# Performance work log

Measured on AMD Instinct MI355X. Metric: run time of the kernel, lower is better.

The kernel has to match this reference:

```python
import jax, jax.numpy as jnp
import numpy as np

B, S, D = 2, 4096, 256
H, DH, DM = 8, 32, 1024
ROPE_BASE = 10000.0
LN_EPS = 1e-5


def _layer_norm(x, g, b):
    mu = jnp.mean(x, axis=-1, keepdims=True)
    var = jnp.mean(jnp.square(x - mu), axis=-1, keepdims=True)
    return (x - mu) * jax.lax.rsqrt(var + LN_EPS) * g + b


def _rope(x):
    # x: [b, s, h, d_head]; lucidrains interleaved-pair RoPE
    s, d = x.shape[1], x.shape[-1]
    inv_freq = 1.0 / (ROPE_BASE ** (jnp.arange(0, d, 2, dtype=jnp.float32) / d))  # [d/2]
    freqs = jnp.arange(s, dtype=jnp.float32)[:, None] * inv_freq[None, :]          # [s, d/2]
    freqs = jnp.repeat(freqs, 2, axis=-1)                                          # [s, d]
    cos = jnp.cos(freqs)[None, :, None, :]
    sin = jnp.sin(freqs)[None, :, None, :]
    x1, x2 = x[..., 0::2], x[..., 1::2]
    rot = jnp.stack((-x2, x1), axis=-1).reshape(x.shape)
    return x * cos + rot * sin


def setup_inputs() -> dict:
    key = jax.random.key(0)
    ks = jax.random.split(key, 8)
    sw = 1.0 / np.sqrt(D)
    return {
        "x": jax.random.normal(ks[0], (B, S, D), jnp.float32),
        "Wq": jax.random.normal(ks[1], (D, D), jnp.float32) * sw,
        "Wk": jax.random.normal(ks[2], (D, D), jnp.float32) * sw,
        "Wv": jax.random.normal(ks[3], (D, D), jnp.float32) * sw,
        "Wo": jax.random.normal(ks[4], (D, D), jnp.float32) * sw,
        "ln1_g": jnp.ones((D,), jnp.float32),
        "ln1_b": jnp.zeros((D,), jnp.float32),
        "ln2_g": jnp.ones((D,), jnp.float32),
        "ln2_b": jnp.zeros((D,), jnp.float32),
        "W2": jax.random.normal(ks[5], (DM, D), jnp.float32) * sw,
        "b2": jnp.zeros((DM,), jnp.float32),
        "W3": jax.random.normal(ks[6], (D, DM), jnp.float32) * (1.0 / np.sqrt(DM)),
        "b3": jnp.zeros((D,), jnp.float32),
    }


def reference(x, Wq, Wk, Wv, Wo, ln1_g, ln1_b, ln2_g, ln2_b, W2, b2, W3, b3):
    b, s, d = x.shape
    h, dh = H, DH
    xn = _layer_norm(x, ln1_g, ln1_b)
    q = (xn @ Wq.T).reshape(b, s, h, dh)
    k = (xn @ Wk.T).reshape(b, s, h, dh)
    v = (xn @ Wv.T).reshape(b, s, h, dh)
    q = _rope(q)
    k = _rope(k)
    # scores: [b, h, q, k] (full matrix, matching original implementation)
    scores = jnp.einsum('bqhd,bkhd->bhqk', q, k) / np.sqrt(dh)
    attn = jax.nn.softmax(scores, axis=-1)
    out = jnp.einsum('bhqk,bkhd->bqhd', attn, v).reshape(b, s, d)
    out = out @ Wo.T
    mlp_in = out + x
    y = _layer_norm(mlp_in, ln2_g, ln2_b)
    y = jax.nn.gelu(y @ W2.T + b2, approximate=False)
    y = y @ W3.T + b3
    return y + mlp_in
```

## Files before the change

### kernel.cpp

```cpp
#include <hip/hip_runtime.h>
#include <math.h>

#define D 256
#define S 4096
#define H 8
#define DH 32
#define DM 1024
#define NTOK 8192

typedef __attribute__((ext_vector_type(8))) short short8;
typedef __attribute__((ext_vector_type(4))) float f32x4;

#define QSCALE (0.17677669529663687f * 1.4426950408889634f)

__device__ inline unsigned short f2bf(float f) {
    union { float f; unsigned u; } v; v.f = f;
    unsigned r = v.u + 0x7fffu + ((v.u >> 16) & 1u);
    return (unsigned short)(r >> 16);
}
__device__ inline void gload16(const void* g, void* l) {
    __builtin_amdgcn_global_load_lds((const __attribute__((address_space(1))) void*)g,
                                     (__attribute__((address_space(3))) void*)l, 16, 0, 0);
}

__global__ void prep(const float* __restrict__ Wq, const float* __restrict__ Wk,
                     const float* __restrict__ Wv, const float* __restrict__ Wo,
                     const float* __restrict__ W2, const float* __restrict__ W3,
                     unsigned short* __restrict__ wqkv, unsigned short* __restrict__ wo_b,
                     unsigned short* __restrict__ w2_b, unsigned short* __restrict__ w3_b,
                     float* __restrict__ ct, float* __restrict__ st,
                     const float* __restrict__ x, const float* __restrict__ g,
                     const float* __restrict__ b, unsigned short* __restrict__ xn) {
    int blk = blockIdx.x;
    if (blk < 3328) {
        int i = blk * 256 + threadIdx.x;
        if (i < 196608) {
            const float* s = (i < 65536) ? Wq : ((i < 131072) ? Wk : Wv);
            wqkv[i] = f2bf(s[i & 65535]);
        } else if (i < 262144) {
            wo_b[i - 196608] = f2bf(Wo[i - 196608]);
        } else if (i < 524288) {
            w2_b[i - 262144] = f2bf(W2[i - 262144]);
        } else if (i < 786432) {
            w3_b[i - 524288] = f2bf(W3[i - 524288]);
        } else {
            int j = i - 786432;
            int spos = j >> 4, pi = j & 15;
            float inv_freq = powf(10000.0f, -(float)(2 * pi) / 32.0f);
            float fr = (float)spos * inv_freq;
            ct[j] = cosf(fr);
            st[j] = sinf(fr);
        }
        return;
    }
    int l = threadIdx.x & 63;
    int row = (blk - 3328) * 4 + (threadIdx.x >> 6);
    const float4 v = *(const float4*)(x + (size_t)row * D + l * 4);
    float s  = v.x + v.y + v.z + v.w;
    float s2 = v.x * v.x + v.y * v.y + v.z * v.z + v.w * v.w;
    #pragma unroll
    for (int off = 32; off > 0; off >>= 1) {
        s  += __shfl_xor(s, off, 64);
        s2 += __shfl_xor(s2, off, 64);
    }
    float mu  = s * (1.0f / D);
    float var = s2 * (1.0f / D) - mu * mu;
    float rs  = rsqrtf(var + 1e-5f);
    const float4 gg = *(const float4*)(g + l * 4);
    const float4 bb = *(const float4*)(b + l * 4);
    ushort4 o;
    o.x = f2bf((v.x - mu) * rs * gg.x + bb.x);
    o.y = f2bf((v.y - mu) * rs * gg.y + bb.y);
    o.z = f2bf((v.z - mu) * rs * gg.z + bb.z);
    o.w = f2bf((v.w - mu) * rs * gg.w + bb.w);
    *(ushort4*)(xn + (size_t)row * D + l * 4) = o;
}

__global__ void ln_kernel(const float* __restrict__ x, const float* __restrict__ g,
                          const float* __restrict__ b, unsigned short* __restrict__ out) {
    int l = threadIdx.x & 63;
    int row = blockIdx.x * 4 + (threadIdx.x >> 6);
    const float4 v = *(const float4*)(x + (size_t)row * D + l * 4);
    float s  = v.x + v.y + v.z + v.w;
    float s2 = v.x * v.x + v.y * v.y + v.z * v.z + v.w * v.w;
    #pragma unroll
    for (int off = 32; off > 0; off >>= 1) {
        s  += __shfl_xor(s, off, 64);
        s2 += __shfl_xor(s2, off, 64);
    }
    float mu  = s * (1.0f / D);
    float var = s2 * (1.0f / D) - mu * mu;
    float rs  = rsqrtf(var + 1e-5f);
    const float4 gg = *(const float4*)(g + l * 4);
    const float4 bb = *(const float4*)(b + l * 4);
    ushort4 o;
    o.x = f2bf((v.x - mu) * rs * gg.x + bb.x);
    o.y = f2bf((v.y - mu) * rs * gg.y + bb.y);
    o.z = f2bf((v.z - mu) * rs * gg.z + bb.z);
    o.w = f2bf((v.w - mu) * rs * gg.w + bb.w);
    *(ushort4*)(out + (size_t)row * D + l * 4) = o;
}

__global__ __launch_bounds__(256) void gemm64b(const unsigned short* __restrict__ A,
        const unsigned short* __restrict__ Bw, void* __restrict__ outp,
        unsigned short* __restrict__ vt,
        const float* __restrict__ bias,
        const float* __restrict__ ct, const float* __restrict__ st,
        int N, int K, int mode) {
    __shared__ unsigned short As[2][64 * 64];
    __shared__ unsigned short Bs[2][64 * 64];
    int tid = threadIdx.x;
    int w = tid >> 6, l = tid & 63;
    int lm = l & 15, lg = l >> 4;
    int wm = (w >> 1) * 32, wn = (w & 1) * 32;
    int bm = blockIdx.x * 64, bn = blockIdx.y * 64;
    int r1 = tid >> 3, pc = tid & 7;
    int pcx = (pc ^ (r1 & 7)) * 8;
    const unsigned short* Ag1 = A + (size_t)(bm + r1) * K + pcx;
    const unsigned short* Ag2 = A + (size_t)(bm + 32 + r1) * K + pcx;
    const unsigned short* Bg1 = Bw + (size_t)(bn + r1) * K + pcx;
    const unsigned short* Bg2 = Bw + (size_t)(bn + 32 + r1) * K + pcx;
    const int swz = lm & 7;
    f32x4 acc[2][2] = {};

    gload16(Ag1, &As[0][w * 512]);
    gload16(Ag2, &As[0][2048 + w * 512]);
    gload16(Bg1, &Bs[0][w * 512]);
    gload16(Bg2, &Bs[0][2048 + w * 512]);
    for (int k0 = 0; k0 < K; k0 += 64) {
        int cur = (k0 >> 6) & 1;
        __syncthreads();
        if (k0 + 64 < K) {
            gload16(Ag1 + k0 + 64, &As[1 - cur][w * 512]);
            gload16(Ag2 + k0 + 64, &As[1 - cur][2048 + w * 512]);
            gload16(Bg1 + k0 + 64, &Bs[1 - cur][w * 512]);
            gload16(Bg2 + k0 + 64, &Bs[1 - cur][2048 + w * 512]);
        }
        #pragma unroll
        for (int j = 0; j < 2; ++j) {
            int ch = ((j * 4 + lg) ^ swz) * 8;
            short8 af[2], bf[2];
            #pragma unroll
            for (int i = 0; i < 2; ++i) af[i] = *(const short8*)&As[cur][(wm + i * 16 + lm) * 64 + ch];
            #pragma unroll
            for (int i = 0; i < 2; ++i) bf[i] = *(const short8*)&Bs[cur][(wn + i * 16 + lm) * 64 + ch];
            #pragma unroll
            for (int mi = 0; mi < 2; ++mi)
                #pragma unroll
                for (int ni = 0; ni < 2; ++ni)
                    acc[mi][ni] = __builtin_amdgcn_mfma_f32_16x16x32_bf16(af[mi], bf[ni], acc[mi][ni], 0, 0, 0);
        }
    }

    if (mode == 0) {
        if (bn >= 512) {
            #pragma unroll
            for (int mi = 0; mi < 2; ++mi) {
                #pragma unroll
                for (int ni = 0; ni < 2; ++ni) {
                    int ng = bn + wn + ni * 16 + lm - 512;
                    int hh = ng >> 5, dh = ng & 31;
                    int mg0 = bm + wm + mi * 16 + lg * 4;
                    int bb = mg0 >> 12, ss = mg0 & 4095;
                    ushort4 pv;
                    pv.x = f2bf(acc[mi][ni][0]); pv.y = f2bf(acc[mi][ni][1]);
                    pv.z = f2bf(acc[mi][ni][2]); pv.w = f2bf(acc[mi][ni][3]);
                    *(ushort4*)(vt + ((size_t)((bb * 8 + hh) * 32 + dh)) * S + ss) = pv;
                }
            }
        } else {
            #pragma unroll
            for (int mi = 0; mi < 2; ++mi) {
                #pragma unroll
                for (int ni = 0; ni < 2; ++ni) {
                    int ng = bn + wn + ni * 16 + lm;
                    int pi = (ng & 31) >> 1;
                    float sgn = (ng & 1) ? 1.f : -1.f;
                    float qs  = (ng < 256) ? QSCALE : 1.f;
                    #pragma unroll
                    for (int r2 = 0; r2 < 4; ++r2) {
                        int mg = bm + wm + mi * 16 + lg * 4 + r2;
                        int spos = mg & (S - 1);
                        float vv = acc[mi][ni][r2];
                        float pv = __shfl_xor(vv, 1, 64);
                        float cs = ct[spos * 16 + pi];
                        float sn = st[spos * 16 + pi];
                        float ov = (vv * cs + sgn * pv * sn) * qs;
                        ((unsigned short*)outp)[(size_t)mg * N + ng] = f2bf(ov);
                    }
                }
            }
        }
        return;
    }
    #pragma unroll
    for (int mi = 0; mi < 2; ++mi) {
        #pragma unroll
        for (int ni = 0; ni < 2; ++ni) {
            int ng = bn + wn + ni * 16 + lm;
            #pragma unroll
            for (int r2 = 0; r2 < 4; ++r2) {
                int mg = bm + wm + mi * 16 + lg * 4 + r2;
                float t = acc[mi][ni][r2] + bias[ng];
                ((unsigned short*)outp)[(size_t)mg * N + ng] =
                    f2bf(0.5f * t * (1.0f + erff(t * 0.70710678118654752f)));
            }
        }
    }
}

__global__ __launch_bounds__(256) void gemm32(const unsigned short* __restrict__ A,
        const unsigned short* __restrict__ Bw, void* __restrict__ outp,
        const float* __restrict__ bias, const float* __restrict__ res,
        int N, int K, int mode) {
    __shared__ unsigned short As[2][32 * 128];
    __shared__ unsigned short Bs[2][64 * 128];
    int tid = threadIdx.x;
    int w = tid >> 6, l = tid & 63;
    int lm = l & 15, lg = l >> 4;
    int rm = (w >> 1) * 16, wn = (w & 1) * 32;
    int bm = blockIdx.x * 32, bn = blockIdx.y * 64;
    int r1 = tid >> 4, pc = tid & 15;
    int pcx = (pc ^ (r1 & 7)) * 8;
    const unsigned short* Ag1 = A + (size_t)(bm + r1) * K + pcx;
    const unsigned short* Ag2 = A + (size_t)(bm + 16 + r1) * K + pcx;
    const unsigned short* Bg1 = Bw + (size_t)(bn + r1) * K + pcx;
    const unsigned short* Bg2 = Bw + (size_t)(bn + 16 + r1) * K + pcx;
    const unsigned short* Bg3 = Bw + (size_t)(bn + 32 + r1) * K + pcx;
    const unsigned short* Bg4 = Bw + (size_t)(bn + 48 + r1) * K + pcx;
    const int swz = lm & 7;
    f32x4 acc[2] = {};

    gload16(Ag1, &As[0][w * 512]);
    gload16(Ag2, &As[0][2048 + w * 512]);
    gload16(Bg1, &Bs[0][w * 512]);
    gload16(Bg2, &Bs[0][2048 + w * 512]);
    gload16(Bg3, &Bs[0][4096 + w * 512]);
    gload16(Bg4, &Bs[0][6144 + w * 512]);
    for (int k0 = 0; k0 < K; k0 += 128) {
        int cur = (k0 >> 7) & 1;
        __syncthreads();
        if (k0 + 128 < K) {
            gload16(Ag1 + k0 + 128, &As[1 - cur][w * 512]);
            gload16(Ag2 + k0 + 128, &As[1 - cur][2048 + w * 512]);
            gload16(Bg1 + k0 + 128, &Bs[1 - cur][w * 512]);
            gload16(Bg2 + k0 + 128, &Bs[1 - cur][2048 + w * 512]);
            gload16(Bg3 + k0 + 128, &Bs[1 - cur][4096 + w * 512]);
            gload16(Bg4 + k0 + 128, &Bs[1 - cur][6144 + w * 512]);
        }
        #pragma unroll
        for (int j = 0; j < 4; ++j) {
            int ch = ((j * 4 + lg) ^ swz) * 8;
            short8 af = *(const short8*)&As[cur][(rm + lm) * 128 + ch];
            short8 bf[2];
            #pragma unroll
            for (int i = 0; i < 2; ++i) bf[i] = *(const short8*)&Bs[cur][(wn + i * 16 + lm) * 128 + ch];
            #pragma unroll
            for (int ni = 0; ni < 2; ++ni)
                acc[ni] = __builtin_amdgcn_mfma_f32_16x16x32_bf16(af, bf[ni], acc[ni], 0, 0, 0);
        }
    }

    #pragma unroll
    for (int ni = 0; ni < 2; ++ni) {
        int ng = bn + wn + ni * 16 + lm;
        #pragma unroll
        for (int r2 = 0; r2 < 4; ++r2) {
            int mg = bm + rm + lg * 4 + r2;
            float v = acc[ni][r2];
            size_t idx = (size_t)mg * N + ng;
            if (mode == 1) {
                ((float*)outp)[idx] = v + res[idx];
            } else {
                ((float*)outp)[idx] = v + bias[ng] + res[idx];
            }
        }
    }
}

__global__ __launch_bounds__(512) void attn_kernel(const unsigned short* __restrict__ Cq,
        const unsigned short* __restrict__ vt, unsigned short* __restrict__ out) {
    __shared__ unsigned short Ks[2][2][64][32];
    __shared__ unsigned short Vs[2][2][32][64];
    __shared__ unsigned short Ones[16][64];
    int tid = threadIdx.x;
    int w = tid >> 6, l = tid & 63;
    int grp = w >> 2, ws = w & 3;
    int lm = l & 15, lg = l >> 4;
    int qt = blockIdx.x >> 4;
    int bh = blockIdx.x & 15;
    int bb = bh >> 3, h = bh & 7;
    int q0 = qt * 64 + ws * 16;

    if (tid < 256) {
        unsigned short val = (tid < 16) ? (unsigned short)0x3F80 : (unsigned short)0;
        *(ushort4*)(&Ones[0][0] + tid * 4) = make_ushort4(val, val, val, val);
    }

    const short8 qf = *(const short8*)(Cq + ((size_t)(bb * S + q0 + lm)) * 768 + h * DH + lg * 8);
    int p = ws * 16 + (l >> 2);
    int krow = ((p >> 5) << 5) + (((p >> 2) & 3) << 3) + (((p >> 4) & 1) << 2) + (p & 3);
    const unsigned short* kg = Cq + ((size_t)(bb * S)) * 768 + 256 + h * 32
                               + (size_t)krow * 768 + ((l & 3) ^ ((l >> 3) & 3)) * 8;
    const unsigned short* vg = vt + ((size_t)(bh * 32 + ws * 8 + (l >> 3))) * S + ((l & 7) ^ (l >> 3)) * 8;
    const int kswz = (lm >> 1) & 3;
    const int vswz = lm & 7;

    f32x4 o0 = {0.f, 0.f, 0.f, 0.f}, o1 = {0.f, 0.f, 0.f, 0.f}, o2 = {0.f, 0.f, 0.f, 0.f};
    const f32x4 z = {0.f, 0.f, 0.f, 0.f};

    gload16(kg + (size_t)grp * 64 * 768, &Ks[grp][0][ws * 16][0]);
    gload16(vg + (size_t)grp * 64,       &Vs[grp][0][ws * 8][0]);

    #pragma unroll 2
    for (int it = 0; it < S / 128; ++it) {
        int cur = it & 1;
        __syncthreads();
        if (it + 1 < S / 128) {
            size_t t = (size_t)(2 * (it + 1) + grp);
            gload16(kg + t * 64 * 768, &Ks[grp][1 - cur][ws * 16][0]);
            gload16(vg + t * 64,       &Vs[grp][1 - cur][ws * 8][0]);
        }
        #pragma unroll
        for (int half = 0; half < 2; ++half) {
            short8 kf0 = *(const short8*)&Ks[grp][cur][half * 32 + lm][(lg ^ kswz) * 8];
            short8 kf1 = *(const short8*)&Ks[grp][cur][half * 32 + 16 + lm][(lg ^ kswz) * 8];
            f32x4 s0 = __builtin_amdgcn_mfma_f32_16x16x32_bf16(kf0, qf, z, 0, 0, 0);
            f32x4 s1 = __builtin_amdgcn_mfma_f32_16x16x32_bf16(kf1, qf, z, 0, 0, 0);
            unsigned u0[4], u1[4];
            #pragma unroll
            for (int i = 0; i < 4; ++i) {
                union { float f; unsigned u; } c0, c1;
                c0.f = __builtin_amdgcn_exp2f(s0[i]);
                c1.f = __builtin_amdgcn_exp2f(s1[i]);
                u0[i] = c0.u;
                u1[i] = c1.u;
            }
            union { unsigned u[4]; short8 s; } pk;
            pk.u[0] = __builtin_amdgcn_perm(u0[1], u0[0], 0x07060302u);
            pk.u[1] = __builtin_amdgcn_perm(u0[3], u0[2], 0x07060302u);
            pk.u[2] = __builtin_amdgcn_perm(u1[1], u1[0], 0x07060302u);
            pk.u[3] = __builtin_amdgcn_perm(u1[3], u1[2], 0x07060302u);
            short8 pf = pk.s;
            int vc = ((half * 4 + lg) ^ vswz) * 8;
            short8 va0 = *(const short8*)&Vs[grp][cur][lm][vc];
            short8 va1 = *(const short8*)&Vs[grp][cur][16 + lm][vc];
            short8 va2 = *(const short8*)&Ones[lm][vc];
            o0 = __builtin_amdgcn_mfma_f32_16x16x32_bf16(va0, pf, o0, 0, 0, 0);
            o1 = __builtin_amdgcn_mfma_f32_16x16x32_bf16(va1, pf, o1, 0, 0, 0);
            o2 = __builtin_amdgcn_mfma_f32_16x16x32_bf16(va2, pf, o2, 0, 0, 0);
        }
    }
    f32x4* Red0 = (f32x4*)&Ks[1][0][0][0];
    f32x4* Red1 = (f32x4*)&Vs[1][0][0][0];
    float* Den  = (float*)&Ones[0][0];
    __syncthreads();
    if (grp) {
        Red0[ws * 64 + l] = o0;
        Red1[ws * 64 + l] = o1;
        Den[ws * 64 + l]  = o2[0];
    }
    __syncthreads();
    if (!grp) {
        f32x4 a0 = Red0[ws * 64 + l];
        f32x4 a1 = Red1[ws * 64 + l];
        float dd = o2[0] + Den[ws * 64 + l];
        #pragma unroll
        for (int i = 0; i < 4; ++i) { o0[i] += a0[i]; o1[i] += a1[i]; }
        float lsum = __shfl(dd, lm, 64);
        float inv = 1.0f / lsum;
        ushort4 r0, r1;
        r0.x = f2bf(o0[0] * inv); r0.y = f2bf(o0[1] * inv);
        r0.z = f2bf(o0[2] * inv); r0.w = f2bf(o0[3] * inv);
        r1.x = f2bf(o1[0] * inv); r1.y = f2bf(o1[1] * inv);
        r1.z = f2bf(o1[2] * inv); r1.w = f2bf(o1[3] * inv);
        unsigned short* ob = out + ((size_t)(bb * S + q0 + lm)) * D + h * DH;
        *(ushort4*)(ob + lg * 4)      = r0;
        *(ushort4*)(ob + 16 + lg * 4) = r1;
    }
}

extern "C" void kernel_launch(void* const* d_in, const int* in_sizes, int n_in,
                              void* d_out, int out_size, void* d_ws, size_t ws_size,
                              hipStream_t stream) {
    const float* x     = (const float*)d_in[0];
    const float* Wq    = (const float*)d_in[1];
    const float* Wk    = (const float*)d_in[2];
    const float* Wv    = (const float*)d_in[3];
    const float* Wo    = (const float*)d_in[4];
    const float* ln1_g = (const float*)d_in[5];
    const float* ln1_b = (const float*)d_in[6];
    const float* ln2_g = (const float*)d_in[7];
    const float* ln2_b = (const float*)d_in[8];
    const float* W2    = (const float*)d_in[9];
    const float* b2    = (const float*)d_in[10];
    const float* W3    = (const float*)d_in[11];
    const float* b3    = (const float*)d_in[12];

    char* w8 = (char*)d_ws;
    unsigned short* wqkv = (unsigned short*)(w8);
    unsigned short* wo_b = (unsigned short*)(w8 + 393216);
    unsigned short* w2_b = (unsigned short*)(w8 + 524288);
    unsigned short* w3_b = (unsigned short*)(w8 + 1048576);
    float*          ct   = (float*)(w8 + 1572864);
    float*          st   = (float*)(w8 + 1835008);
    unsigned short* xn   = (unsigned short*)(w8 + 2097152);
    unsigned short* Cq   = (unsigned short*)(w8 + 6291456);
    unsigned short* hb   = Cq;
    unsigned short* vtb  = (unsigned short*)(w8 + 23068672);
    unsigned short* ab   = (unsigned short*)(w8 + 27262976);
    float*          mlpin= (float*)(w8 + 31457280);
    unsigned short* yn   = xn;

    prep<<<5376, 256, 0, stream>>>(Wq, Wk, Wv, Wo, W2, W3, wqkv, wo_b, w2_b, w3_b,
                                   ct, st, x, ln1_g, ln1_b, xn);
    gemm64b<<<dim3(128, 12), 256, 0, stream>>>(xn, wqkv, Cq, vtb, nullptr, ct, st, 768, 256, 0);
    attn_kernel<<<1024, 512, 0, stream>>>(Cq, vtb, ab);
    gemm32<<<dim3(256, 4), 256, 0, stream>>>(ab, wo_b, mlpin, nullptr, x, 256, 256, 1);
    ln_kernel<<<NTOK / 4, 256, 0, stream>>>(mlpin, ln2_g, ln2_b, yn);
    gemm64b<<<dim3(128, 16), 256, 0, stream>>>(yn, w2_b, hb, nullptr, b2, nullptr, nullptr, 1024, 256, 2);
    gemm32<<<dim3(256, 4), 256, 0, stream>>>(hb, w3_b, (float*)d_out, b3, mlpin, 256, 1024, 3);
}
```

Baseline: 197.1 us.

## Process two query tiles per wave in attention to reuse K/V fragments

Each attention wave now handles 32 query rows instead of 16, reusing each K and V fragment loaded from shared memory for two score and PV MFMA chains. This halves the grid to 512 blocks and the total K/V global traffic. The ones-matrix used for the row-sum denominator is built in registers instead of being read from LDS. The cost is more registers per wave, with a launch-bounds occupancy hint added, and fewer blocks to spread across CUs.

```diff
diff --git a/kernel.cpp b/kernel.cpp
--- a/kernel.cpp
+++ b/kernel.cpp
@@ -21,6 +21,24 @@
 __device__ inline void gload16(const void* g, void* l) {
     __builtin_amdgcn_global_load_lds((const __attribute__((address_space(1))) void*)g,
                                      (__attribute__((address_space(3))) void*)l, 16, 0, 0);
+}
+
+__device__ inline short8 pack_p(f32x4 s0, f32x4 s1) {
+    unsigned u0[4], u1[4];
+    #pragma unroll
+    for (int i = 0; i < 4; ++i) {
+        union { float f; unsigned u; } c0, c1;
+        c0.f = __builtin_amdgcn_exp2f(s0[i]);
+        c1.f = __builtin_amdgcn_exp2f(s1[i]);
+        u0[i] = c0.u;
+        u1[i] = c1.u;
+    }
+    union { unsigned u[4]; short8 s; } pk;
+    pk.u[0] = __builtin_amdgcn_perm(u0[1], u0[0], 0x07060302u);
+    pk.u[1] = __builtin_amdgcn_perm(u0[3], u0[2], 0x07060302u);
+    pk.u[2] = __builtin_amdgcn_perm(u1[1], u1[0], 0x07060302u);
+    pk.u[3] = __builtin_amdgcn_perm(u1[3], u1[2], 0x07060302u);
+    return pk.s;
 }
 
 __global__ void prep(const float* __restrict__ Wq, const float* __restrict__ Wk,
@@ -278,11 +296,10 @@
     }
 }
 
-__global__ __launch_bounds__(512) void attn_kernel(const unsigned short* __restrict__ Cq,
+__global__ __launch_bounds__(512, 4) void attn_kernel(const unsigned short* __restrict__ Cq,
         const unsigned short* __restrict__ vt, unsigned short* __restrict__ out) {
     __shared__ unsigned short Ks[2][2][64][32];
     __shared__ unsigned short Vs[2][2][32][64];
-    __shared__ unsigned short Ones[16][64];
     int tid = threadIdx.x;
     int w = tid >> 6, l = tid & 63;
     int grp = w >> 2, ws = w & 3;
@@ -290,14 +307,19 @@
     int qt = blockIdx.x >> 4;
     int bh = blockIdx.x & 15;
     int bb = bh >> 3, h = bh & 7;
-    int q0 = qt * 64 + ws * 16;
-
-    if (tid < 256) {
-        unsigned short val = (tid < 16) ? (unsigned short)0x3F80 : (unsigned short)0;
-        *(ushort4*)(&Ones[0][0] + tid * 4) = make_ushort4(val, val, val, val);
-    }
-
-    const short8 qf = *(const short8*)(Cq + ((size_t)(bb * S + q0 + lm)) * 768 + h * DH + lg * 8);
+    int q0 = qt * 128 + ws * 32;
+
+    const short8 qfa = *(const short8*)(Cq + ((size_t)(bb * S + q0 + lm)) * 768 + h * DH + lg * 8);
+    const short8 qfb = *(const short8*)(Cq + ((size_t)(bb * S + q0 + 16 + lm)) * 768 + h * DH + lg * 8);
+
+    union { unsigned short us[8]; short8 s; } onesu;
+    {
+        unsigned short ov = (lm == 0) ? (unsigned short)0x3F80 : (unsigned short)0;
+        #pragma unroll
+        for (int i = 0; i < 8; ++i) onesu.us[i] = ov;
+    }
+    const short8 onef = onesu.s;
+
     int p = ws * 16 + (l >> 2);
     int krow = ((p >> 5) << 5) + (((p >> 2) & 3) << 3) + (((p >> 4) & 1) << 2) + (p & 3);
     const unsigned short* kg = Cq + ((size_t)(bb * S)) * 768 + 256 + h * 32
@@ -306,7 +328,8 @@
     const int kswz = (lm >> 1) & 3;
     const int vswz = lm & 7;
 
-    f32x4 o0 = {0.f, 0.f, 0.f, 0.f}, o1 = {0.f, 0.f, 0.f, 0.f}, o2 = {0.f, 0.f, 0.f, 0.f};
+    f32x4 o0a = {0.f, 0.f, 0.f, 0.f}, o1a = {0.f, 0.f, 0.f, 0.f}, o2a = {0.f, 0.f, 0.f, 0.f};
+    f32x4 o0b = {0.f, 0.f, 0.f, 0.f}, o1b = {0.f, 0.f, 0.f, 0.f}, o2b = {0.f, 0.f, 0.f, 0.f};
     const f32x4 z = {0.f, 0.f, 0.f, 0.f};
 
     gload16(kg + (size_t)grp * 64 * 768, &Ks[grp][0][ws * 16][0]);
@@ -325,58 +348,64 @@
         for (int half = 0; half < 2; ++half) {
             short8 kf0 = *(const short8*)&Ks[grp][cur][half * 32 + lm][(lg ^ kswz) * 8];
             short8 kf1 = *(const short8*)&Ks[grp][cur][half * 32 + 16 + lm][(lg ^ kswz) * 8];
-            f32x4 s0 = __builtin_amdgcn_mfma_f32_16x16x32_bf16(kf0, qf, z, 0, 0, 0);
-            f32x4 s1 = __builtin_amdgcn_mfma_f32_16x16x32_bf16(kf1, qf, z, 0, 0, 0);
-            unsigned u0[4], u1[4];
-            #pragma unroll
-            for (int i = 0; i < 4; ++i) {
-                union { float f; unsigned u; } c0, c1;
-                c0.f = __builtin_amdgcn_exp2f(s0[i]);
-                c1.f = __builtin_amdgcn_exp2f(s1[i]);
-                u0[i] = c0.u;
-                u1[i] = c1.u;
-            }
-            union { unsigned u[4]; short8 s; } pk;
-            pk.u[0] = __builtin_amdgcn_perm(u0[1], u0[0], 0x07060302u);
-            pk.u[1] = __builtin_amdgcn_perm(u0[3], u0[2], 0x07060302u);
-            pk.u[2] = __builtin_amdgcn_perm(u1[1], u1[0], 0x07060302u);
-            pk.u[3] = __builtin_amdgcn_perm(u1[3], u1[2], 0x07060302u);
-            short8 pf = pk.s;
+            f32x4 s0a = __builtin_amdgcn_mfma_f32_16x16x32_bf16(kf0, qfa, z, 0, 0, 0);
+            f32x4 s1a = __builtin_amdgcn_mfma_f32_16x16x32_bf16(kf1, qfa, z, 0, 0, 0);
+            f32x4 s0b = __builtin_amdgcn_mfma_f32_16x16x32_bf16(kf0, qfb, z, 0, 0, 0);
+            f32x4 s1b = __builtin_amdgcn_mfma_f32_16x16x32_bf16(kf1, qfb, z, 0, 0, 0);
+            short8 pfa = pack_p(s0a, s1a);
+            short8 pfb = pack_p(s0b, s1b);
             int vc = ((half * 4 + lg) ^ vswz) * 8;
             short8 va0 = *(const short8*)&Vs[grp][cur][lm][vc];
             short8 va1 = *(const short8*)&Vs[grp][cur][16 + lm][vc];
-            short8 va2 = *(const short8*)&Ones[lm][vc];
-            o0 = __builtin_amdgcn_mfma_f32_16x16x32_bf16(va0, pf, o0, 0, 0, 0);
-            o1 = __builtin_amdgcn_mfma_f32_16x16x32_bf16(va1, pf, o1, 0, 0, 0);
-            o2 = __builtin_amdgcn_mfma_f32_16x16x32_bf16(va2, pf, o2, 0, 0, 0);
-        }
-    }
-    f32x4* Red0 = (f32x4*)&Ks[1][0][0][0];
-    f32x4* Red1 = (f32x4*)&Vs[1][0][0][0];
-    float* Den  = (float*)&Ones[0][0];
+            o0a = __builtin_amdgcn_mfma_f32_16x16x32_bf16(va0, pfa, o0a, 0, 0, 0);
+            o1a = __builtin_amdgcn_mfma_f32_16x16x32_bf16(va1, pfa, o1a, 0, 0, 0);
+            o2a = __builtin_amdgcn_mfma_f32_16x16x32_bf16(onef, pfa, o2a, 0, 0, 0);
+            o0b = __builtin_amdgcn_mfma_f32_16x16x32_bf16(va0, pfb, o0b, 0, 0, 0);
+            o1b = __builtin_amdgcn_mfma_f32_16x16x32_bf16(va1, pfb, o1b, 0, 0, 0);
+            o2b = __builtin_amdgcn_mfma_f32_16x16x32_bf16(onef, pfb, o2b, 0, 0, 0);
+        }
+    }
+    f32x4* Red = (f32x4*)&Ks[0][0][0][0];
+    float* Den = (float*)&Vs[0][0][0][0];
     __syncthreads();
     if (grp) {
-        Red0[ws * 64 + l] = o0;
-        Red1[ws * 64 + l] = o1;
-        Den[ws * 64 + l]  = o2[0];
+        Red[(0 * 4 + ws) * 64 + l] = o0a;
+        Red[(1 * 4 + ws) * 64 + l] = o1a;
+        Red[(2 * 4 + ws) * 64 + l] = o0b;
+        Red[(3 * 4 + ws) * 64 + l] = o1b;
+        Den[(ws * 2 + 0) * 64 + l] = o2a[0];
+        Den[(ws * 2 + 1) * 64 + l] = o2b[0];
     }
     __syncthreads();
     if (!grp) {
-        f32x4 a0 = Red0[ws * 64 + l];
-        f32x4 a1 = Red1[ws * 64 + l];
-        float dd = o2[0] + Den[ws * 64 + l];
-        #pragma unroll
-        for (int i = 0; i < 4; ++i) { o0[i] += a0[i]; o1[i] += a1[i]; }
-        float lsum = __shfl(dd, lm, 64);
-        float inv = 1.0f / lsum;
+        f32x4 a0 = Red[(0 * 4 + ws) * 64 + l];
+        f32x4 a1 = Red[(1 * 4 + ws) * 64 + l];
+        f32x4 a2 = Red[(2 * 4 + ws) * 64 + l];
+        f32x4 a3 = Red[(3 * 4 + ws) * 64 + l];
+        float dda = o2a[0] + Den[(ws * 2 + 0) * 64 + l];
+        float ddb = o2b[0] + Den[(ws * 2 + 1) * 64 + l];
+        #pragma unroll
+        for (int i = 0; i < 4; ++i) {
+            o0a[i] += a0[i]; o1a[i] += a1[i];
+            o0b[i] += a2[i]; o1b[i] += a3[i];
+        }
+        float inva = 1.0f / __shfl(dda, lm, 64);
+        float invb = 1.0f / __shfl(ddb, lm, 64);
         ushort4 r0, r1;
-        r0.x = f2bf(o0[0] * inv); r0.y = f2bf(o0[1] * inv);
-        r0.z = f2bf(o0[2] * inv); r0.w = f2bf(o0[3] * inv);
-        r1.x = f2bf(o1[0] * inv); r1.y = f2bf(o1[1] * inv);
-        r1.z = f2bf(o1[2] * inv); r1.w = f2bf(o1[3] * inv);
+        r0.x = f2bf(o0a[0] * inva); r0.y = f2bf(o0a[1] * inva);
+        r0.z = f2bf(o0a[2] * inva); r0.w = f2bf(o0a[3] * inva);
+        r1.x = f2bf(o1a[0] * inva); r1.y = f2bf(o1a[1] * inva);
+        r1.z = f2bf(o1a[2] * inva); r1.w = f2bf(o1a[3] * inva);
         unsigned short* ob = out + ((size_t)(bb * S + q0 + lm)) * D + h * DH;
         *(ushort4*)(ob + lg * 4)      = r0;
         *(ushort4*)(ob + 16 + lg * 4) = r1;
+        r0.x = f2bf(o0b[0] * invb); r0.y = f2bf(o0b[1] * invb);
+        r0.z = f2bf(o0b[2] * invb); r0.w = f2bf(o0b[3] * invb);
+        r1.x = f2bf(o1b[0] * invb); r1.y = f2bf(o1b[1] * invb);
+        r1.z = f2bf(o1b[2] * invb); r1.w = f2bf(o1b[3] * invb);
+        unsigned short* ob2 = out + ((size_t)(bb * S + q0 + 16 + lm)) * D + h * DH;
+        *(ushort4*)(ob2 + lg * 4)      = r0;
+        *(ushort4*)(ob2 + 16 + lg * 4) = r1;
     }
 }
 
@@ -415,7 +444,7 @@
     prep<<<5376, 256, 0, stream>>>(Wq, Wk, Wv, Wo, W2, W3, wqkv, wo_b, w2_b, w3_b,
                                    ct, st, x, ln1_g, ln1_b, xn);
     gemm64b<<<dim3(128, 12), 256, 0, stream>>>(xn, wqkv, Cq, vtb, nullptr, ct, st, 768, 256, 0);
-    attn_kernel<<<1024, 512, 0, stream>>>(Cq, vtb, ab);
+    attn_kernel<<<512, 512, 0, stream>>>(Cq, vtb, ab);
     gemm32<<<dim3(256, 4), 256, 0, stream>>>(ab, wo_b, mlpin, nullptr, x, 256, 256, 1);
     ln_kernel<<<NTOK / 4, 256, 0, stream>>>(mlpin, ln2_g, ln2_b, yn);
     gemm64b<<<dim3(128, 16), 256, 0, stream>>>(yn, w2_b, hb, nullptr, b2, nullptr, nullptr, 1024, 256, 2);
```

New measurement: 189.6 us. 3.8% less time.
